# Kernel tuning notes

Measured on AMD Instinct MI355X. Metric: run time of the kernel, lower is better.

The kernel has to match this reference:

```python
import jax, jax.numpy as jnp
import numpy as np

K_NN = 10      # knn_graph(landmarks, 10)
K_HOPS = 2     # TAGConv K
DELTA_T = 10
EPS = 0.1


def knn_edges(pos, k=K_NN):
    # PyG knn_graph with loop=False, flow='source_to_target':
    # edges (src=neighbor j, dst=query i), k nearest excluding self.
    n = pos.shape[0]
    sq = jnp.sum(pos * pos, axis=-1)
    d = sq[:, None] + sq[None, :] - 2.0 * (pos @ pos.T)  # [N,N] squared dists
    d = jnp.where(jnp.eye(n, dtype=bool), jnp.inf, d)
    _, idx = jax.lax.top_k(-d, k)                        # [N,k] neighbor ids
    src = idx.reshape(-1)                                # neighbors (sources)
    dst = jnp.repeat(jnp.arange(n), k)                   # query nodes (targets)
    return src, dst


def tagconv(h, src, dst, conv_ws, conv_b):
    # out = sum_{k=0..K} (A_norm^k h) W_k + b, gcn_norm without self-loops
    n = h.shape[0]
    deg = jax.ops.segment_sum(jnp.ones_like(src, dtype=h.dtype), dst, num_segments=n)
    dinv = jnp.where(deg > 0, jax.lax.rsqrt(deg), 0.0)
    norm = dinv[src] * dinv[dst]                         # [E]
    out = h @ conv_ws[0]
    x = h
    for k in range(1, K_HOPS + 1):
        msg = x[src] * norm[:, None]                     # gather + scale [E,D]
        x = jax.ops.segment_sum(msg, dst, num_segments=n)
        out = out + x @ conv_ws[k]
    return out + conv_b


def setup_inputs() -> dict:
    key = jax.random.key(0)
    ks = jax.random.split(key, 7)
    N, D_IN, D_H, D_OUT = 8192, 3, 256, 3
    s_emb = 1.0 / np.sqrt(D_IN)
    s_h = 1.0 / np.sqrt(D_H)
    return {
        "landmarks": jax.random.normal(ks[0], (N, D_IN), jnp.float32),
        "emb_w": jax.random.normal(ks[1], (D_IN, D_H), jnp.float32) * s_emb,
        "emb_b": jax.random.normal(ks[2], (D_H,), jnp.float32) * 0.01,
        "readout_w": jax.random.normal(ks[3], (D_H, D_OUT), jnp.float32) * s_h,
        "readout_b": jax.random.normal(ks[4], (D_OUT,), jnp.float32) * 0.01,
        "conv_ws": jax.random.normal(ks[5], (K_HOPS + 1, D_H, D_H), jnp.float32) * s_h,
        "conv_b": jax.random.normal(ks[6], (D_H,), jnp.float32) * 0.01,
    }


def reference(landmarks, emb_w, emb_b, readout_w, readout_b, conv_ws, conv_b):
    src, dst = knn_edges(landmarks)
    h = landmarks @ emb_w + emb_b                        # emb
    x = h @ readout_w + readout_b                        # readout of initial state

    def step(hc, _):
        c = tagconv(hc, src, dst, conv_ws, conv_b)
        hn = hc + EPS * jnp.tanh(c)                      # Euler residual step
        return hn, hn @ readout_w + readout_b

    h_final, land_pred = jax.lax.scan(step, h, None, length=DELTA_T)
    y = h_final @ readout_w + readout_b
    return y, h_final, x, land_pred
```

## Files before the change

kernel.cpp:

```cpp
#include <hip/hip_runtime.h>
#include <float.h>
#include <math.h>

#define NN 8192
#define DH 256
#define KNN 10
#define TSTEPS 10
#define EPSC 0.1f
#define CTILE 1024
#define QPB 16

typedef short s8v __attribute__((ext_vector_type(8)));
typedef float f4v __attribute__((ext_vector_type(4)));

__device__ __forceinline__ float bf2f(unsigned short u) {
    union { unsigned u; float f; } c; c.u = ((unsigned)u) << 16; return c.f;
}
__device__ __forceinline__ unsigned short f2bf(float f) {
    union { float f; unsigned u; } c; c.f = f;
    unsigned r = c.u + 0x7FFF + ((c.u >> 16) & 1);
    return (unsigned short)(r >> 16);
}

__global__ void prep_wt(const float* __restrict__ W, unsigned short* __restrict__ Wt) {
    int e = blockIdx.x * 256 + threadIdx.x;
    int g = e >> 16; int rem = e & 65535;
    int n = rem >> 8; int k = rem & 255;
    Wt[e] = f2bf(W[g * 65536 + k * 256 + n]);
}

__global__ void prep_pos(const float* __restrict__ pos, float4* __restrict__ pos4) {
    int j = blockIdx.x * 256 + threadIdx.x;
    float x = pos[j * 3], y = pos[j * 3 + 1], z = pos[j * 3 + 2];
    float4 v; v.x = x; v.y = y; v.z = z; v.w = x * x + y * y + z * z;
    pos4[j] = v;
}

__launch_bounds__(1024)
__global__ void knn_wave(const float* __restrict__ pos, const float4* __restrict__ pos4,
                         int* __restrict__ nbr) {
    __shared__ float4 cand[CTILE];
    int tid = threadIdx.x;
    int wv = tid >> 6, lane = tid & 63;
    int i = blockIdx.x * QPB + wv;
    float xi = pos[i * 3], yi = pos[i * 3 + 1], zi = pos[i * 3 + 2];
    float sqi = xi * xi + yi * yi + zi * zi;
    int igrp = i & ~63;

    float b  = FLT_MAX;
    int   ib = -1;
    float thr = FLT_MAX;

    for (int tile = 0; tile < NN / CTILE; ++tile) {
        __syncthreads();
        cand[tid] = pos4[tile * CTILE + tid];
        __syncthreads();
#pragma unroll 4
        for (int u = 0; u < CTILE / 64; ++u) {
            int jgrp = tile * CTILE + u * 64;
            float4 c = cand[u * 64 + lane];
            int j = jgrp + lane;
            float m = c.x * xi + c.y * yi + c.z * zi;
            float d = (sqi + c.w) - 2.0f * m;
            if (jgrp == igrp) {
                if (j == i) d = FLT_MAX;
            }
            unsigned long long mask = __ballot(d < thr);
            while (mask) {
                int l = __ffsll((unsigned long long)mask) - 1;
                mask &= mask - 1;
                float dc = __int_as_float(__builtin_amdgcn_readlane(__float_as_int(d), l));
                if (dc < thr) {
                    int jc = __builtin_amdgcn_readlane(j, l);
                    float bp = __int_as_float(__builtin_amdgcn_update_dpp(
                        0, __float_as_int(b), 0x111, 0xF, 0xF, true));
                    int ip = __builtin_amdgcn_update_dpp(0, ib, 0x111, 0xF, 0xF, true);
                    bool c0 = dc < b;
                    bool cp = (lane != 0) && (dc < bp);
                    b  = c0 ? (cp ? bp : dc) : b;
                    ib = c0 ? (cp ? ip : jc) : ib;
                    thr = __int_as_float(__builtin_amdgcn_readlane(__float_as_int(b), 9));
                }
            }
        }
    }
    if (lane < KNN) nbr[i * KNN + lane] = ib;
}

__global__ void emb_kernel(const float* __restrict__ lm, const float* __restrict__ ew,
                           const float* __restrict__ eb, const float* __restrict__ rw,
                           const float* __restrict__ rb,
                           float* __restrict__ hdo, unsigned short* __restrict__ hbf,
                           float* __restrict__ xout) {
    __shared__ float s0[4], s1[4], s2[4];
    int i = blockIdx.x, d = threadIdx.x;
    float a0 = lm[i * 3], a1 = lm[i * 3 + 1], a2 = lm[i * 3 + 2];
    float h = eb[d] + a0 * ew[d] + a1 * ew[256 + d] + a2 * ew[512 + d];
    hdo[i * 256 + d] = h;
    hbf[i * 256 + d] = f2bf(h);
    float p0 = h * rw[d * 3], p1 = h * rw[d * 3 + 1], p2 = h * rw[d * 3 + 2];
    for (int off = 32; off; off >>= 1) {
        p0 += __shfl_down(p0, off, 64);
        p1 += __shfl_down(p1, off, 64);
        p2 += __shfl_down(p2, off, 64);
    }
    int lane = d & 63, wid = d >> 6;
    if (lane == 0) { s0[wid] = p0; s1[wid] = p1; s2[wid] = p2; }
    __syncthreads();
    if (d == 0) {
        xout[i * 3 + 0] = s0[0] + s0[1] + s0[2] + s0[3] + rb[0];
        xout[i * 3 + 1] = s1[0] + s1[1] + s1[2] + s1[3] + rb[1];
        xout[i * 3 + 2] = s2[0] + s2[1] + s2[2] + s2[3] + rb[2];
    }
}

__global__ void agg_kernel(const unsigned short* __restrict__ src,
                           unsigned short* __restrict__ dst,
                           const int* __restrict__ nbr) {
    int tid = threadIdx.x;
    int wid = tid >> 6, lane = tid & 63;
    int node = blockIdx.x * 4 + wid;
    int d0 = lane * 4;
    float a0 = 0.f, a1 = 0.f, a2 = 0.f, a3 = 0.f;
    const int* nb = nbr + node * KNN;
    for (int q = 0; q < KNN; q++) {
        int j = nb[q];
        uint2 v = *(const uint2*)(src + j * 256 + d0);
        a0 += bf2f((unsigned short)(v.x & 0xffff));
        a1 += bf2f((unsigned short)(v.x >> 16));
        a2 += bf2f((unsigned short)(v.y & 0xffff));
        a3 += bf2f((unsigned short)(v.y >> 16));
    }
    uint2 o;
    o.x = (unsigned)f2bf(a0 * 0.1f) | ((unsigned)f2bf(a1 * 0.1f) << 16);
    o.y = (unsigned)f2bf(a2 * 0.1f) | ((unsigned)f2bf(a3 * 0.1f) << 16);
    *(uint2*)(dst + node * 256 + d0) = o;
}

__launch_bounds__(256)
__global__ void gemm_step(unsigned short* hbf,
                          const unsigned short* __restrict__ x1,
                          const int* __restrict__ nbr,
                          const unsigned short* __restrict__ Wt,
                          const float* __restrict__ cb,
                          const float* __restrict__ rw, const float* __restrict__ rb,
                          float* hdo, float* __restrict__ yout, float* yfin) {
    __shared__ __align__(16) short Al[16 * 72];
    __shared__ __align__(16) short Bl[256 * 72];
    __shared__ __align__(16) short X2[16 * 264];
    __shared__ float rwl[768];
    __shared__ float cbl[256];
    __shared__ float yred[4][4][4][3];

    int tid = threadIdx.x;
    int m0 = blockIdx.x * 16;
    for (int idx = tid; idx < 768; idx += 256) rwl[idx] = rw[idx];
    cbl[tid] = cb[tid];

    {
        int row = tid >> 4, cg = tid & 15;
        const int* nb = nbr + (m0 + row) * KNN;
        float a[16];
#pragma unroll
        for (int e = 0; e < 16; e++) a[e] = 0.f;
        for (int q = 0; q < KNN; q++) {
            int j = nb[q];
            const uint4* p = (const uint4*)(x1 + j * 256 + cg * 16);
#pragma unroll
            for (int u = 0; u < 2; u++) {
                uint4 v = p[u];
                a[u*8+0] += bf2f((unsigned short)(v.x & 0xffff));
                a[u*8+1] += bf2f((unsigned short)(v.x >> 16));
                a[u*8+2] += bf2f((unsigned short)(v.y & 0xffff));
                a[u*8+3] += bf2f((unsigned short)(v.y >> 16));
                a[u*8+4] += bf2f((unsigned short)(v.z & 0xffff));
                a[u*8+5] += bf2f((unsigned short)(v.z >> 16));
                a[u*8+6] += bf2f((unsigned short)(v.w & 0xffff));
                a[u*8+7] += bf2f((unsigned short)(v.w >> 16));
            }
        }
        unsigned short* xp = (unsigned short*)&X2[row * 264 + cg * 16];
#pragma unroll
        for (int u = 0; u < 2; u++) {
            uint4 o;
            o.x = (unsigned)f2bf(a[u*8+0]*0.1f) | ((unsigned)f2bf(a[u*8+1]*0.1f) << 16);
            o.y = (unsigned)f2bf(a[u*8+2]*0.1f) | ((unsigned)f2bf(a[u*8+3]*0.1f) << 16);
            o.z = (unsigned)f2bf(a[u*8+4]*0.1f) | ((unsigned)f2bf(a[u*8+5]*0.1f) << 16);
            o.w = (unsigned)f2bf(a[u*8+6]*0.1f) | ((unsigned)f2bf(a[u*8+7]*0.1f) << 16);
            *(uint4*)(xp + u * 8) = o;
        }
    }

    f4v acc[4];
    for (int f = 0; f < 4; f++) acc[f] = (f4v){0.f, 0.f, 0.f, 0.f};

    int w = tid >> 6, lane = tid & 63;
    int quad = lane >> 4, l15 = lane & 15;

    for (int kc = 0; kc < 12; kc++) {
        int kb = kc * 64;
        int klocal = kb & 255;
        if (kc < 8 && tid < 128) {
            const unsigned short* asrc = (kb < 256) ? (const unsigned short*)hbf : x1;
            int row = tid >> 3, c8 = (tid & 7) * 8;
            uint4 v = *(const uint4*)(asrc + (m0 + row) * 256 + klocal + c8);
            *(uint4*)(&Al[row * 72 + c8]) = v;
        }
        {
            const unsigned short* bsrc = Wt + (kb >> 8) * 65536;
            int c8 = (tid & 7) * 8, rbase = tid >> 3;
            for (int r2 = 0; r2 < 8; r2++) {
                int n = r2 * 32 + rbase;
                uint4 v = *(const uint4*)(bsrc + n * 256 + klocal + c8);
                *(uint4*)(&Bl[n * 72 + c8]) = v;
            }
        }
        __syncthreads();
        for (int ks = 0; ks < 2; ks++) {
            s8v a;
            if (kc < 8)
                a = *(const s8v*)(&Al[l15 * 72 + ks * 32 + quad * 8]);
            else
                a = *(const s8v*)(&X2[l15 * 264 + klocal + ks * 32 + quad * 8]);
            for (int f = 0; f < 4; f++) {
                int n = w * 64 + f * 16 + l15;
                s8v b = *(const s8v*)(&Bl[n * 72 + ks * 32 + quad * 8]);
                acc[f] = __builtin_amdgcn_mfma_f32_16x16x32_bf16(a, b, acc[f], 0, 0, 0);
            }
        }
        __syncthreads();
    }

    float py[4][3] = {};
    for (int f = 0; f < 4; f++) {
        int col = w * 64 + f * 16 + l15;
        float cbv = cbl[col];
        float rw0 = rwl[col * 3], rw1 = rwl[col * 3 + 1], rw2 = rwl[col * 3 + 2];
        for (int r = 0; r < 4; r++) {
            int grow = m0 + quad * 4 + r;
            float cval = acc[f][r] + cbv;
            float hn = hdo[grow * 256 + col] + EPSC * tanhf(cval);
            hdo[grow * 256 + col] = hn;
            hbf[grow * 256 + col] = f2bf(hn);
            py[r][0] += hn * rw0; py[r][1] += hn * rw1; py[r][2] += hn * rw2;
        }
    }
    for (int off = 1; off < 16; off <<= 1)
        for (int r = 0; r < 4; r++)
            for (int j = 0; j < 3; j++)
                py[r][j] += __shfl_xor(py[r][j], off, 64);
    if (l15 == 0)
        for (int r = 0; r < 4; r++)
            for (int j = 0; j < 3; j++)
                yred[w][quad][r][j] = py[r][j];
    __syncthreads();
    if (w == 0 && l15 == 0) {
        for (int r = 0; r < 4; r++) {
            int grow = m0 + quad * 4 + r;
            for (int j = 0; j < 3; j++) {
                float yv = yred[0][quad][r][j] + yred[1][quad][r][j]
                         + yred[2][quad][r][j] + yred[3][quad][r][j] + rb[j];
                yout[grow * 3 + j] = yv;
                if (yfin) yfin[grow * 3 + j] = yv;
            }
        }
    }
}

extern "C" void kernel_launch(void* const* d_in, const int* in_sizes, int n_in,
                              void* d_out, int out_size, void* d_ws, size_t ws_size,
                              hipStream_t stream) {
    const float* lm = (const float*)d_in[0];
    const float* ew = (const float*)d_in[1];
    const float* eb = (const float*)d_in[2];
    const float* rw = (const float*)d_in[3];
    const float* rb = (const float*)d_in[4];
    const float* cw = (const float*)d_in[5];
    const float* cb = (const float*)d_in[6];

    float* out = (float*)d_out;
    float* y_out = out;
    float* h_out = out + 24576;
    float* x_out = out + 24576 + 2097152;
    float* lp_out = x_out + 24576;

    char* ws = (char*)d_ws;
    int* nbr = (int*)ws;                       ws += NN * KNN * sizeof(int);
    float4* pos4 = (float4*)ws;                ws += NN * sizeof(float4);
    char* uni = ws;
    unsigned short* hbf = (unsigned short*)uni;
    unsigned short* x1  = hbf + NN * DH;
    unsigned short* Wt  = x1 + NN * DH;

    prep_pos<<<NN / 256, 256, 0, stream>>>(lm, pos4);
    knn_wave<<<NN / QPB, 1024, 0, stream>>>(lm, pos4, nbr);
    prep_wt<<<768, 256, 0, stream>>>(cw, Wt);
    emb_kernel<<<NN, 256, 0, stream>>>(lm, ew, eb, rw, rb, h_out, hbf, x_out);
    for (int t = 0; t < TSTEPS; t++) {
        agg_kernel<<<NN / 4, 256, 0, stream>>>(hbf, x1, nbr);
        gemm_step<<<NN / 16, 256, 0, stream>>>(hbf, x1, nbr, Wt, cb, rw, rb, h_out,
                                               lp_out + t * 24576,
                                               (t == TSTEPS - 1) ? y_out : nullptr);
    }
}
```

Measured before the change: 435.4 us.

## Enlarge gemm_step tile to 32 rows with 1024 threads and double-buffered weights

Each gemm_step block now handles 32 rows using 16 waves instead of 16 rows with 4 waves. Weight K-chunks are double-buffered in LDS with register prefetch, which removes one barrier per chunk. The full hbf row tile is staged into LDS once, so each weight chunk load is reused across twice as many rows. This halves the number of blocks to 256, which may underfill the GPU, and 1024-thread blocks with larger LDS use can lower occupancy.

```diff
diff --git a/kernel.cpp b/kernel.cpp
--- a/kernel.cpp
+++ b/kernel.cpp
@@ -137,7 +137,7 @@
     *(uint2*)(dst + node * 256 + d0) = o;
 }
 
-__launch_bounds__(256)
+__launch_bounds__(1024)
 __global__ void gemm_step(unsigned short* hbf,
                           const unsigned short* __restrict__ x1,
                           const int* __restrict__ nbr,
@@ -145,99 +145,110 @@
                           const float* __restrict__ cb,
                           const float* __restrict__ rw, const float* __restrict__ rb,
                           float* hdo, float* __restrict__ yout, float* yfin) {
-    __shared__ __align__(16) short Al[16 * 72];
-    __shared__ __align__(16) short Bl[256 * 72];
-    __shared__ __align__(16) short X2[16 * 264];
+    __shared__ __align__(16) short Al[32 * 264];
+    __shared__ __align__(16) short X2[32 * 264];
+    __shared__ __align__(16) short Bl[2][256 * 72];
     __shared__ float rwl[768];
     __shared__ float cbl[256];
-    __shared__ float yred[4][4][4][3];
+    __shared__ float yred[16][4][4][3];
 
     int tid = threadIdx.x;
-    int m0 = blockIdx.x * 16;
-    for (int idx = tid; idx < 768; idx += 256) rwl[idx] = rw[idx];
-    cbl[tid] = cb[tid];
+    int m0 = blockIdx.x * 32;
+    if (tid < 768) rwl[tid] = rw[tid];
+    if (tid < 256) cbl[tid] = cb[tid];
+
+    int w = tid >> 6, lane = tid & 63;
+    int quad = lane >> 4, l15 = lane & 15;
+    int rt = w >> 3, cfg = w & 7;
+
+    int arow = tid >> 5, acg = tid & 31;
+    int bn = tid >> 2, bk = (tid & 3) * 16;
 
     {
-        int row = tid >> 4, cg = tid & 15;
-        const int* nb = nbr + (m0 + row) * KNN;
-        float a[16];
-#pragma unroll
-        for (int e = 0; e < 16; e++) a[e] = 0.f;
+        const int* nb = nbr + (m0 + arow) * KNN;
+        float a[8];
+#pragma unroll
+        for (int e = 0; e < 8; e++) a[e] = 0.f;
         for (int q = 0; q < KNN; q++) {
             int j = nb[q];
-            const uint4* p = (const uint4*)(x1 + j * 256 + cg * 16);
-#pragma unroll
-            for (int u = 0; u < 2; u++) {
-                uint4 v = p[u];
-                a[u*8+0] += bf2f((unsigned short)(v.x & 0xffff));
-                a[u*8+1] += bf2f((unsigned short)(v.x >> 16));
-                a[u*8+2] += bf2f((unsigned short)(v.y & 0xffff));
-                a[u*8+3] += bf2f((unsigned short)(v.y >> 16));
-                a[u*8+4] += bf2f((unsigned short)(v.z & 0xffff));
-                a[u*8+5] += bf2f((unsigned short)(v.z >> 16));
-                a[u*8+6] += bf2f((unsigned short)(v.w & 0xffff));
-                a[u*8+7] += bf2f((unsigned short)(v.w >> 16));
+            uint4 v = *(const uint4*)(x1 + j * 256 + acg * 8);
+            a[0] += bf2f((unsigned short)(v.x & 0xffff));
+            a[1] += bf2f((unsigned short)(v.x >> 16));
+            a[2] += bf2f((unsigned short)(v.y & 0xffff));
+            a[3] += bf2f((unsigned short)(v.y >> 16));
+            a[4] += bf2f((unsigned short)(v.z & 0xffff));
+            a[5] += bf2f((unsigned short)(v.z >> 16));
+            a[6] += bf2f((unsigned short)(v.w & 0xffff));
+            a[7] += bf2f((unsigned short)(v.w >> 16));
+        }
+        uint4 o;
+        o.x = (unsigned)f2bf(a[0]*0.1f) | ((unsigned)f2bf(a[1]*0.1f) << 16);
+        o.y = (unsigned)f2bf(a[2]*0.1f) | ((unsigned)f2bf(a[3]*0.1f) << 16);
+        o.z = (unsigned)f2bf(a[4]*0.1f) | ((unsigned)f2bf(a[5]*0.1f) << 16);
+        o.w = (unsigned)f2bf(a[6]*0.1f) | ((unsigned)f2bf(a[7]*0.1f) << 16);
+        *(uint4*)((unsigned short*)&X2[arow * 264 + acg * 8]) = o;
+    }
+
+    {
+        uint4 va = *(const uint4*)(((const unsigned short*)hbf) + (m0 + arow) * 256 + acg * 8);
+        *(uint4*)((unsigned short*)&Al[arow * 264 + acg * 8]) = va;
+        uint4 v0 = *(const uint4*)(Wt + bn * 256 + bk);
+        uint4 v1 = *(const uint4*)(Wt + bn * 256 + bk + 8);
+        *(uint4*)(&Bl[0][bn * 72 + bk]) = v0;
+        *(uint4*)(&Bl[0][bn * 72 + bk + 8]) = v1;
+    }
+    __syncthreads();
+
+    f4v acc[2];
+    acc[0] = (f4v){0.f, 0.f, 0.f, 0.f};
+    acc[1] = (f4v){0.f, 0.f, 0.f, 0.f};
+
+#pragma unroll
+    for (int kc = 0; kc < 12; kc++) {
+        const int cur = kc & 1;
+        uint4 v0, v1;
+        if (kc + 1 < 12) {
+            const unsigned short* bsrc = Wt + ((kc + 1) >> 2) * 65536 + ((kc + 1) & 3) * 64;
+            v0 = *(const uint4*)(bsrc + bn * 256 + bk);
+            v1 = *(const uint4*)(bsrc + bn * 256 + bk + 8);
+        }
+        uint4 va;
+        if (kc == 3)
+            va = *(const uint4*)(x1 + (m0 + arow) * 256 + acg * 8);
+        {
+            const short* Abase = (kc < 8) ? Al : X2;
+            int kl = (kc & 3) * 64;
+#pragma unroll
+            for (int ks = 0; ks < 2; ks++) {
+                s8v a = *(const s8v*)(&Abase[(rt * 16 + l15) * 264 + kl + ks * 32 + quad * 8]);
+#pragma unroll
+                for (int f = 0; f < 2; f++) {
+                    int n = (cfg * 2 + f) * 16 + l15;
+                    s8v b = *(const s8v*)(&Bl[cur][n * 72 + ks * 32 + quad * 8]);
+                    acc[f] = __builtin_amdgcn_mfma_f32_16x16x32_bf16(a, b, acc[f], 0, 0, 0);
+                }
             }
         }
-        unsigned short* xp = (unsigned short*)&X2[row * 264 + cg * 16];
-#pragma unroll
-        for (int u = 0; u < 2; u++) {
-            uint4 o;
-            o.x = (unsigned)f2bf(a[u*8+0]*0.1f) | ((unsigned)f2bf(a[u*8+1]*0.1f) << 16);
-            o.y = (unsigned)f2bf(a[u*8+2]*0.1f) | ((unsigned)f2bf(a[u*8+3]*0.1f) << 16);
-            o.z = (unsigned)f2bf(a[u*8+4]*0.1f) | ((unsigned)f2bf(a[u*8+5]*0.1f) << 16);
-            o.w = (unsigned)f2bf(a[u*8+6]*0.1f) | ((unsigned)f2bf(a[u*8+7]*0.1f) << 16);
-            *(uint4*)(xp + u * 8) = o;
-        }
-    }
-
-    f4v acc[4];
-    for (int f = 0; f < 4; f++) acc[f] = (f4v){0.f, 0.f, 0.f, 0.f};
-
-    int w = tid >> 6, lane = tid & 63;
-    int quad = lane >> 4, l15 = lane & 15;
-
-    for (int kc = 0; kc < 12; kc++) {
-        int kb = kc * 64;
-        int klocal = kb & 255;
-        if (kc < 8 && tid < 128) {
-            const unsigned short* asrc = (kb < 256) ? (const unsigned short*)hbf : x1;
-            int row = tid >> 3, c8 = (tid & 7) * 8;
-            uint4 v = *(const uint4*)(asrc + (m0 + row) * 256 + klocal + c8);
-            *(uint4*)(&Al[row * 72 + c8]) = v;
-        }
-        {
-            const unsigned short* bsrc = Wt + (kb >> 8) * 65536;
-            int c8 = (tid & 7) * 8, rbase = tid >> 3;
-            for (int r2 = 0; r2 < 8; r2++) {
-                int n = r2 * 32 + rbase;
-                uint4 v = *(const uint4*)(bsrc + n * 256 + klocal + c8);
-                *(uint4*)(&Bl[n * 72 + c8]) = v;
-            }
+        if (kc + 1 < 12) {
+            *(uint4*)(&Bl[cur ^ 1][bn * 72 + bk]) = v0;
+            *(uint4*)(&Bl[cur ^ 1][bn * 72 + bk + 8]) = v1;
         }
         __syncthreads();
-        for (int ks = 0; ks < 2; ks++) {
-            s8v a;
-            if (kc < 8)
-                a = *(const s8v*)(&Al[l15 * 72 + ks * 32 + quad * 8]);
-            else
-                a = *(const s8v*)(&X2[l15 * 264 + klocal + ks * 32 + quad * 8]);
-            for (int f = 0; f < 4; f++) {
-                int n = w * 64 + f * 16 + l15;
-                s8v b = *(const s8v*)(&Bl[n * 72 + ks * 32 + quad * 8]);
-                acc[f] = __builtin_amdgcn_mfma_f32_16x16x32_bf16(a, b, acc[f], 0, 0, 0);
-            }
-        }
-        __syncthreads();
+        if (kc == 3) {
+            *(uint4*)((unsigned short*)&Al[arow * 264 + acg * 8]) = va;
+            __syncthreads();
+        }
     }
 
     float py[4][3] = {};
-    for (int f = 0; f < 4; f++) {
-        int col = w * 64 + f * 16 + l15;
+#pragma unroll
+    for (int f = 0; f < 2; f++) {
+        int col = (cfg * 2 + f) * 16 + l15;
         float cbv = cbl[col];
         float rw0 = rwl[col * 3], rw1 = rwl[col * 3 + 1], rw2 = rwl[col * 3 + 2];
+#pragma unroll
         for (int r = 0; r < 4; r++) {
-            int grow = m0 + quad * 4 + r;
+            int grow = m0 + rt * 16 + quad * 4 + r;
             float cval = acc[f][r] + cbv;
             float hn = hdo[grow * 256 + col] + EPSC * tanhf(cval);
             hdo[grow * 256 + col] = hn;
@@ -255,13 +266,16 @@
                 yred[w][quad][r][j] = py[r][j];
     __syncthreads();
     if (w == 0 && l15 == 0) {
-        for (int r = 0; r < 4; r++) {
-            int grow = m0 + quad * 4 + r;
-            for (int j = 0; j < 3; j++) {
-                float yv = yred[0][quad][r][j] + yred[1][quad][r][j]
-                         + yred[2][quad][r][j] + yred[3][quad][r][j] + rb[j];
-                yout[grow * 3 + j] = yv;
-                if (yfin) yfin[grow * 3 + j] = yv;
+        for (int rt2 = 0; rt2 < 2; rt2++) {
+            for (int r = 0; r < 4; r++) {
+                int grow = m0 + rt2 * 16 + quad * 4 + r;
+                for (int j = 0; j < 3; j++) {
+                    float yv = rb[j];
+                    for (int ww = rt2 * 8; ww < rt2 * 8 + 8; ww++)
+                        yv += yred[ww][quad][r][j];
+                    yout[grow * 3 + j] = yv;
+                    if (yfin) yfin[grow * 3 + j] = yv;
+                }
             }
         }
     }
@@ -298,8 +312,8 @@
     emb_kernel<<<NN, 256, 0, stream>>>(lm, ew, eb, rw, rb, h_out, hbf, x_out);
     for (int t = 0; t < TSTEPS; t++) {
         agg_kernel<<<NN / 4, 256, 0, stream>>>(hbf, x1, nbr);
-        gemm_step<<<NN / 16, 256, 0, stream>>>(hbf, x1, nbr, Wt, cb, rw, rb, h_out,
-                                               lp_out + t * 24576,
-                                               (t == TSTEPS - 1) ? y_out : nullptr);
-    }
-}
+        gemm_step<<<NN / 32, 1024, 0, stream>>>(hbf, x1, nbr, Wt, cb, rw, rb, h_out,
+                                                lp_out + t * 24576,
+                                                (t == TSTEPS - 1) ? y_out : nullptr);
+    }
+}
```

Result: faster. 398.8 us (-8.4%).
